# Performance work log

Hardware: AMD Instinct MI355X
Metric: run time of the kernel (lower is better)

The kernel has to match this reference:

```python
import jax, jax.numpy as jnp
import numpy as np

K = 20
EPS = 1e-5
NEG_SLOPE = 0.2


def knn_idx(x, k):
    # x: [B, C, N]; returns indices of k nearest neighbors [B, N, k]
    xx = jnp.sum(x * x, axis=1)                      # [B, N]
    inner = jnp.einsum('bcn,bcm->bnm', x, x)         # [B, N, N]
    neg_dist = 2.0 * inner - xx[:, :, None] - xx[:, None, :]
    return jax.lax.top_k(neg_dist, k)[1]             # [B, N, k]


def graph_feature(x, k):
    # x: [B, C, N] -> [B, 2C, N, k]
    idx = knn_idx(x, k)
    xT = jnp.transpose(x, (0, 2, 1))                 # [B, N, C]
    nbrs = jax.vmap(lambda feats, ids: feats[ids])(xT, idx)   # [B, N, k, C]
    ctr = jnp.broadcast_to(xT[:, :, None, :], nbrs.shape)
    feat = jnp.concatenate([nbrs - ctr, ctr], axis=-1)        # [B, N, k, 2C]
    return jnp.transpose(feat, (0, 3, 1, 2))


def bn(x, g, b, axes):
    # training-mode batchnorm over `axes`, channel dim = 1
    m = jnp.mean(x, axis=axes, keepdims=True)
    v = jnp.var(x, axis=axes, keepdims=True)
    shape = [1] * x.ndim
    shape[1] = -1
    g = g.reshape(shape)
    b = b.reshape(shape)
    return g * (x - m) * jax.lax.rsqrt(v + EPS) + b


def lrelu(x):
    return jax.nn.leaky_relu(x, NEG_SLOPE)


def setup_inputs() -> dict:
    key = jax.random.key(0)
    ks = jax.random.split(key, 4)
    x = jax.random.normal(ks[0], (4, 16, 512, 3), dtype=jnp.float32)
    w1 = jax.random.normal(ks[1], (64, 6), dtype=jnp.float32) * 0.1
    w2 = jax.random.normal(ks[2], (256, 128), dtype=jnp.float32) * 0.05
    w3 = jax.random.normal(ks[3], (512, 320), dtype=jnp.float32) * 0.05
    ones = jnp.ones
    zeros = jnp.zeros
    return {
        'x': x,
        'w1': w1, 'g1': ones(64, jnp.float32), 'b1': zeros(64, jnp.float32),
        'w2': w2, 'g2': ones(256, jnp.float32), 'b2': zeros(256, jnp.float32),
        'w3': w3, 'g3': ones(512, jnp.float32), 'b3': zeros(512, jnp.float32),
    }


def reference(x, w1, g1, b1, w2, g2, b2, w3, g3, b3):
    B, P, N, D = x.shape
    xp = jnp.transpose(x.reshape(B * P, N, D), (0, 2, 1))    # [BP, 3, N]

    f = graph_feature(xp, K)                                  # [BP, 6, N, K]
    h = lrelu(bn(jnp.einsum('bcnk,oc->bonk', f, w1), g1, b1, (0, 2, 3)))
    x1 = jnp.max(h, axis=-1)                                  # [BP, 64, N]

    f = graph_feature(x1, K)                                  # [BP, 128, N, K]
    h = lrelu(bn(jnp.einsum('bcnk,oc->bonk', f, w2), g2, b2, (0, 2, 3)))
    x2 = jnp.max(h, axis=-1)                                  # [BP, 256, N]

    cat = jnp.concatenate([x1, x2], axis=1)                   # [BP, 320, N]
    h = lrelu(bn(jnp.einsum('bcn,oc->bon', cat, w3), g3, b3, (0, 2)))  # [BP, 512, N]

    pooled = jnp.concatenate([jnp.max(h, axis=-1), jnp.mean(h, axis=-1)], axis=1)  # [BP, 1024]
    return pooled.reshape(B, P, -1)
```

## Files before the change

### kernel.cpp

```cpp
#include <hip/hip_runtime.h>
#include <hip/hip_bf16.h>
#include <math.h>

#define NBP 64
#define NP  512
#define KK  20

using short8 = __attribute__((ext_vector_type(8))) short;
using f32x4  = __attribute__((ext_vector_type(4))) float;

constexpr size_t O_X1   = 0;
constexpr size_t O_XCH  = 8388608;
constexpr size_t O_XCL  = 29360128;
constexpr size_t O_D    = 50331648;
constexpr size_t O_IDX  = 117440512;
constexpr size_t O_XX2  = 120061952;
constexpr size_t O_WC   = 120193024;
constexpr size_t O_W3H  = 120324096;
constexpr size_t O_W3L  = 120651776;
constexpr size_t O_SC1  = 120979456;
constexpr size_t O_SC2  = 120979968;
constexpr size_t O_SC3  = 120982016;
constexpr size_t O_ST1  = 120986112;
constexpr size_t O_ST2  = 120994304;
constexpr size_t O_ST3  = 121125376;
constexpr size_t STATS_BYTES = 8192 + 131072 + 262144;

__global__ __launch_bounds__(256) void prepw_kernel(const float* __restrict__ w2,
                                                    const float* __restrict__ w3,
                                                    float* __restrict__ Wcat,
                                                    __hip_bfloat16* __restrict__ w3h,
                                                    __hip_bfloat16* __restrict__ w3l) {
    int i = blockIdx.x * 256 + threadIdx.x;
    if (i < 32768) {
        int c = i >> 9, q = i & 511;
        Wcat[i] = (q < 256) ? w2[q * 128 + c]
                            : (w2[(q - 256) * 128 + 64 + c] - w2[(q - 256) * 128 + c]);
    } else if (i < 32768 + 163840) {
        int j = i - 32768;
        float v = w3[j];
        __hip_bfloat16 h = __float2bfloat16(v);
        w3h[j] = h;
        w3l[j] = __float2bfloat16(v - __bfloat162float(h));
    }
}

__device__ __forceinline__ void wave_top20_set(const float v[8], int lane, int* __restrict__ outp) {
    unsigned u[8];
#pragma unroll
    for (int q = 0; q < 8; q++) {
        unsigned b = __float_as_uint(v[q]);
        u[q] = (b & 0x80000000u) ? ~b : (b | 0x80000000u);
    }
    unsigned T = 0u;
    for (int b = 31; b >= 0; b--) {
        unsigned cand = T | (1u << b);
        int cnt = 0;
#pragma unroll
        for (int q = 0; q < 8; q++)
            cnt += __popcll(__ballot(u[q] >= cand));
        if (cnt >= KK) T = cand;
    }
    unsigned long long lmask = (1ull << lane) - 1ull;
    int slotbase = 0;
#pragma unroll
    for (int q = 0; q < 8; q++) {
        unsigned long long bgt = __ballot(u[q] > T);
        if (u[q] > T) {
            int slot = slotbase + __popcll(bgt & lmask);
            outp[slot] = lane + (q << 6);
        }
        slotbase += __popcll(bgt);
    }
    int need = KK - slotbase;
#pragma unroll
    for (int q = 0; q < 8; q++) {
        if (need > 0) {
            unsigned long long beq = __ballot(u[q] == T);
            int cq = __popcll(beq);
            int take = need < cq ? need : cq;
            if (u[q] == T) {
                int p = __popcll(beq & lmask);
                if (p < take) outp[slotbase + p] = lane + (q << 6);
            }
            slotbase += take;
            need -= take;
        }
    }
}

__global__ __launch_bounds__(256) void knn1_kernel(const float* __restrict__ x, int* __restrict__ idx1) {
    __shared__ float px[NP * 3];
    __shared__ float sxx[NP];
    int bp = blockIdx.x >> 7;
    int pg = blockIdx.x & 127;
    int wid = threadIdx.x >> 6;
    int lane = threadIdx.x & 63;
    int n = pg * 4 + wid;
    const float* xb = x + (size_t)bp * NP * 3;
    for (int i = threadIdx.x; i < NP * 3; i += 256) px[i] = xb[i];
    __syncthreads();
    for (int i = threadIdx.x; i < NP; i += 256) {
        float a = px[i * 3], b = px[i * 3 + 1], c = px[i * 3 + 2];
        sxx[i] = a * a + b * b + c * c;
    }
    __syncthreads();
    float rn0 = px[n * 3], rn1 = px[n * 3 + 1], rn2 = px[n * 3 + 2];
    float xxn = sxx[n];
    float v[8];
#pragma unroll
    for (int q = 0; q < 8; q++) {
        int m = lane + (q << 6);
        float dot = rn0 * px[m * 3] + rn1 * px[m * 3 + 1] + rn2 * px[m * 3 + 2];
        v[q] = 2.0f * dot - xxn - sxx[m];
    }
    wave_top20_set(v, lane, idx1 + ((size_t)bp * NP + n) * KK);
}

__global__ __launch_bounds__(256) void conv1_kernel(const float* __restrict__ x, const float* __restrict__ w1,
                                                    const int* __restrict__ idx1,
                                                    float* __restrict__ h1max, float* __restrict__ h1min,
                                                    double* __restrict__ stats1) {
    __shared__ double red1[4][64][2];
    int bp = blockIdx.x >> 5;
    int nt = blockIdx.x & 31;
    int n0 = nt * 16;
    int o  = threadIdx.x & 63;
    int nq = threadIdx.x >> 6;
    const float* xb = x + (size_t)bp * NP * 3;
    float w[6];
#pragma unroll
    for (int c = 0; c < 6; c++) w[c] = w1[o * 6 + c];
    double s = 0.0, s2 = 0.0;
    float omx[4], omn[4];
#pragma unroll
    for (int nn = 0; nn < 4; nn++) {
        int n = n0 + nq * 4 + nn;
        float c0 = xb[n * 3], c1 = xb[n * 3 + 1], c2 = xb[n * 3 + 2];
        const int* ip = idx1 + ((size_t)bp * NP + n) * KK;
        float mx = -INFINITY, mn = INFINITY;
        for (int k = 0; k < KK; k++) {
            int j = ip[k];
            float e0 = xb[j * 3], e1 = xb[j * 3 + 1], e2 = xb[j * 3 + 2];
            float h = w[0] * (e0 - c0) + w[1] * (e1 - c1) + w[2] * (e2 - c2)
                    + w[3] * c0 + w[4] * c1 + w[5] * c2;
            mx = fmaxf(mx, h); mn = fminf(mn, h);
            s += (double)h; s2 += (double)h * (double)h;
        }
        omx[nn] = mx; omn[nn] = mn;
    }
    size_t base = ((size_t)bp * 64 + o) * NP + n0 + nq * 4;
    *(float4*)&h1max[base] = make_float4(omx[0], omx[1], omx[2], omx[3]);
    *(float4*)&h1min[base] = make_float4(omn[0], omn[1], omn[2], omn[3]);
    red1[nq][o][0] = s; red1[nq][o][1] = s2;
    __syncthreads();
    if (threadIdx.x < 64) {
        int oo = threadIdx.x;
        double S = 0, S2 = 0;
        for (int q = 0; q < 4; q++) { S += red1[q][oo][0]; S2 += red1[q][oo][1]; }
        int copy = blockIdx.x & 7;
        atomicAdd(&stats1[(copy * 64 + oo) * 2], S);
        atomicAdd(&stats1[(copy * 64 + oo) * 2 + 1], S2);
    }
}

__global__ __launch_bounds__(256) void fprep_kernel(const double* __restrict__ stats, int ncopy, int nch,
                                                    double invN, const float* __restrict__ g,
                                                    const float* __restrict__ b, float* __restrict__ scsh) {
    int o = blockIdx.x * 256 + threadIdx.x;
    if (o >= nch) return;
    double S = 0, S2 = 0;
    for (int c = 0; c < ncopy; c++) {
        S  += stats[((size_t)c * nch + o) * 2];
        S2 += stats[((size_t)c * nch + o) * 2 + 1];
    }
    double m = S * invN;
    double v = S2 * invN - m * m;
    double sc = (double)g[o] / sqrt(v + 1e-5);
    scsh[o * 2]     = (float)sc;
    scsh[o * 2 + 1] = (float)((double)b[o] - sc * m);
}

__global__ __launch_bounds__(256) void fin1_kernel(const float* __restrict__ h1max, const float* __restrict__ h1min,
                                                   const float* __restrict__ scsh,
                                                   float* __restrict__ x1,
                                                   __hip_bfloat16* __restrict__ XCh,
                                                   __hip_bfloat16* __restrict__ XCl) {
    __shared__ float tile[64][33];
    int bp = blockIdx.x >> 4, nt = blockIdx.x & 15, n0 = nt * 32;
    for (int i = threadIdx.x; i < 64 * 32; i += 256) {
        int o = i >> 5, nl = i & 31;
        float sc = scsh[o * 2], sh = scsh[o * 2 + 1];
        size_t gi = ((size_t)bp * 64 + o) * NP + n0 + nl;
        float v = (sc >= 0.0f) ? h1max[gi] : h1min[gi];
        float y = sc * v + sh;
        y = (y >= 0.0f) ? y : 0.2f * y;
        x1[gi] = y;
        tile[o][nl] = y;
    }
    __syncthreads();
    for (int i = threadIdx.x; i < 64 * 32; i += 256) {
        int nl = i >> 6, o = i & 63;
        float y = tile[o][nl];
        __hip_bfloat16 h = __float2bfloat16(y);
        size_t base = ((size_t)bp * NP + n0 + nl) * 320 + o;
        XCh[base] = h;
        XCl[base] = __float2bfloat16(y - __bfloat162float(h));
    }
}

__global__ __launch_bounds__(256) void xx2_kernel(const float* __restrict__ x1, float* __restrict__ xx2v) {
    int i = blockIdx.x * 256 + threadIdx.x;
    int bp = i >> 9, n = i & 511;
    const float* xb = x1 + (size_t)bp * 64 * NP + n;
    float acc = 0.0f;
    for (int c = 0; c < 64; c++) { float v = xb[c * NP]; acc += v * v; }
    xx2v[i] = acc;
}

__global__ __launch_bounds__(256) void gram_kernel(const float* __restrict__ x1, const float* __restrict__ xx2v,
                                                   float* __restrict__ Dm) {
    __shared__ float An[64 * 128];
    __shared__ float Bm[64 * 128];
    int bp = blockIdx.x >> 4;
    int ntb = (blockIdx.x >> 2) & 3, mtb = blockIdx.x & 3;
    int n0 = ntb * 128, m0 = mtb * 128;
    const float* xb = x1 + (size_t)bp * 64 * NP;
    for (int i = threadIdx.x; i < 64 * 128; i += 256) {
        int c = i >> 7, r = i & 127;
        An[i] = xb[c * NP + n0 + r];
        Bm[i] = xb[c * NP + m0 + r];
    }
    __syncthreads();
    int ng = threadIdx.x & 15, mg = threadIdx.x >> 4;
    float acc[8][8];
#pragma unroll
    for (int r = 0; r < 8; r++)
#pragma unroll
        for (int j = 0; j < 8; j++) acc[r][j] = 0.0f;
    const float* ap = An + ng * 8;
    const float* bq = Bm + mg * 8;
#pragma unroll 2
    for (int c = 0; c < 64; c++) {
        float4 a0 = *(const float4*)(ap + c * 128);
        float4 a1 = *(const float4*)(ap + c * 128 + 4);
        float4 b0 = *(const float4*)(bq + c * 128);
        float4 b1 = *(const float4*)(bq + c * 128 + 4);
        float av[8] = {a0.x, a0.y, a0.z, a0.w, a1.x, a1.y, a1.z, a1.w};
        float bv[8] = {b0.x, b0.y, b0.z, b0.w, b1.x, b1.y, b1.z, b1.w};
#pragma unroll
        for (int r = 0; r < 8; r++)
#pragma unroll
            for (int j = 0; j < 8; j++) acc[r][j] += av[r] * bv[j];
    }
    float xm[8];
#pragma unroll
    for (int j = 0; j < 8; j++) xm[j] = xx2v[bp * NP + m0 + mg * 8 + j];
#pragma unroll
    for (int r = 0; r < 8; r++) {
        float xxn = xx2v[bp * NP + n0 + ng * 8 + r];
        float out[8];
#pragma unroll
        for (int j = 0; j < 8; j++) out[j] = 2.0f * acc[r][j] - xxn - xm[j];
        size_t base = ((size_t)bp * NP + n0 + ng * 8 + r) * NP + m0 + mg * 8;
        *(float4*)&Dm[base]     = make_float4(out[0], out[1], out[2], out[3]);
        *(float4*)&Dm[base + 4] = make_float4(out[4], out[5], out[6], out[7]);
    }
}

__global__ __launch_bounds__(256) void topk2_kernel(const float* __restrict__ Dm, int* __restrict__ idx2) {
    int wid = threadIdx.x >> 6;
    int lane = threadIdx.x & 63;
    int row = blockIdx.x * 4 + wid;
    const float* dr = Dm + (size_t)row * NP;
    float v[8];
#pragma unroll
    for (int q = 0; q < 8; q++) v[q] = dr[lane + (q << 6)];
    wave_top20_set(v, lane, idx2 + (size_t)row * KK);
}

__global__ __launch_bounds__(256) void conv2a_kernel(const float* __restrict__ x1, const float* __restrict__ Wcat,
                                                     float* __restrict__ Aout, float* __restrict__ Dtout) {
    __shared__ float An[64 * 128];
    __shared__ float Bm[64 * 128];
    int bp = blockIdx.x >> 4;
    int ntb = (blockIdx.x >> 2) & 3, qtb = blockIdx.x & 3;
    int n0 = ntb * 128, q0 = qtb * 128;
    const float* xb = x1 + (size_t)bp * 64 * NP;
    for (int i = threadIdx.x; i < 64 * 128; i += 256) {
        int c = i >> 7, r = i & 127;
        An[i] = xb[c * NP + n0 + r];
        Bm[i] = Wcat[c * 512 + q0 + r];
    }
    __syncthreads();
    int ng = threadIdx.x & 15, mg = threadIdx.x >> 4;
    float acc[8][8];
#pragma unroll
    for (int r = 0; r < 8; r++)
#pragma unroll
        for (int j = 0; j < 8; j++) acc[r][j] = 0.0f;
    const float* ap = An + ng * 8;
    const float* bq = Bm + mg * 8;
#pragma unroll 2
    for (int c = 0; c < 64; c++) {
        float4 a0 = *(const float4*)(ap + c * 128);
        float4 a1 = *(const float4*)(ap + c * 128 + 4);
        float4 b0 = *(const float4*)(bq + c * 128);
        float4 b1 = *(const float4*)(bq + c * 128 + 4);
        float av[8] = {a0.x, a0.y, a0.z, a0.w, a1.x, a1.y, a1.z, a1.w};
        float bv[8] = {b0.x, b0.y, b0.z, b0.w, b1.x, b1.y, b1.z, b1.w};
#pragma unroll
        for (int r = 0; r < 8; r++)
#pragma unroll
            for (int j = 0; j < 8; j++) acc[r][j] += av[r] * bv[j];
    }
    float* ob = (q0 < 256) ? Aout : Dtout;
    int qoff = (q0 & 255) + mg * 8;
#pragma unroll
    for (int r = 0; r < 8; r++) {
        size_t base = ((size_t)bp * NP + n0 + ng * 8 + r) * 256 + qoff;
        *(float4*)&ob[base]     = make_float4(acc[r][0], acc[r][1], acc[r][2], acc[r][3]);
        *(float4*)&ob[base + 4] = make_float4(acc[r][4], acc[r][5], acc[r][6], acc[r][7]);
    }
}

__global__ __launch_bounds__(256) void conv2b_kernel(const float* __restrict__ A, const float* __restrict__ Dt,
                                                     const int* __restrict__ idx2,
                                                     double* __restrict__ stats2) {
    __shared__ float Al[512 * 16];
    __shared__ double red[16][16][2];
    int bid = blockIdx.x;
    int bp = bid >> 5;
    int ot = (bid >> 1) & 15, nh = bid & 1;
    int o0 = ot * 16, n0 = nh * 256;
    int tid = threadIdx.x;
    for (int i = tid; i < 2048; i += 256) {
        int j = i >> 2, p = i & 3;
        *(float4*)&Al[j * 16 + p * 4] = *(const float4*)&A[((size_t)bp * NP + j) * 256 + o0 + p * 4];
    }
    __syncthreads();
    int o = tid & 15, np = tid >> 4;
    double sh = 0.0, sh2 = 0.0;
    for (int nn = 0; nn < 16; nn++) {
        int n = n0 + np * 16 + nn;
        const int* ip = idx2 + ((size_t)bp * NP + n) * KK;
        int4 ia = *(const int4*)ip, ib = *(const int4*)(ip + 4), ic = *(const int4*)(ip + 8);
        int4 id4 = *(const int4*)(ip + 12), ie = *(const int4*)(ip + 16);
        int js[20] = {ia.x, ia.y, ia.z, ia.w, ib.x, ib.y, ib.z, ib.w, ic.x, ic.y, ic.z, ic.w,
                      id4.x, id4.y, id4.z, id4.w, ie.x, ie.y, ie.z, ie.w};
        float dv = Dt[((size_t)bp * NP + n) * 256 + o0 + o];
        float s1 = 0.0f, s2 = 0.0f;
#pragma unroll
        for (int k = 0; k < KK; k++) {
            float a = Al[js[k] * 16 + o];
            s1 += a; s2 += a * a;
        }
        sh  += (double)s1 + 20.0 * (double)dv;
        sh2 += (double)s2 + 2.0 * (double)dv * (double)s1 + 20.0 * (double)dv * (double)dv;
    }
    red[np][o][0] = sh; red[np][o][1] = sh2;
    __syncthreads();
    if (tid < 16) {
        double S = 0, S2 = 0;
        for (int q = 0; q < 16; q++) { S += red[q][tid][0]; S2 += red[q][tid][1]; }
        int copy = bid & 31;
        atomicAdd(&stats2[(copy * 256 + o0 + tid) * 2], S);
        atomicAdd(&stats2[(copy * 256 + o0 + tid) * 2 + 1], S2);
    }
}

__global__ __launch_bounds__(256) void fin2g_kernel(const float* __restrict__ A, const float* __restrict__ Dt,
                                                    const int* __restrict__ idx2,
                                                    const float* __restrict__ scsh,
                                                    __hip_bfloat16* __restrict__ XCh,
                                                    __hip_bfloat16* __restrict__ XCl) {
    __shared__ float Al[512 * 16];
    int bid = blockIdx.x;
    int bp = bid >> 5;
    int ot = (bid >> 1) & 15, nh = bid & 1;
    int o0 = ot * 16, n0 = nh * 256;
    int tid = threadIdx.x;
    for (int i = tid; i < 2048; i += 256) {
        int j = i >> 2, p = i & 3;
        *(float4*)&Al[j * 16 + p * 4] = *(const float4*)&A[((size_t)bp * NP + j) * 256 + o0 + p * 4];
    }
    __syncthreads();
    int o = tid & 15, np = tid >> 4;
    float sc = scsh[(o0 + o) * 2], shift = scsh[(o0 + o) * 2 + 1];
    for (int nn = 0; nn < 16; nn++) {
        int n = n0 + np * 16 + nn;
        const int* ip = idx2 + ((size_t)bp * NP + n) * KK;
        int4 ia = *(const int4*)ip, ib = *(const int4*)(ip + 4), ic = *(const int4*)(ip + 8);
        int4 id4 = *(const int4*)(ip + 12), ie = *(const int4*)(ip + 16);
        int js[20] = {ia.x, ia.y, ia.z, ia.w, ib.x, ib.y, ib.z, ib.w, ic.x, ic.y, ic.z, ic.w,
                      id4.x, id4.y, id4.z, id4.w, ie.x, ie.y, ie.z, ie.w};
        float dv = Dt[((size_t)bp * NP + n) * 256 + o0 + o];
        float mx = -INFINITY, mn = INFINITY;
#pragma unroll
        for (int k = 0; k < KK; k++) {
            float a = Al[js[k] * 16 + o];
            mx = fmaxf(mx, a); mn = fminf(mn, a);
        }
        float v = ((sc >= 0.0f) ? mx : mn) + dv;
        float y = sc * v + shift;
        y = (y >= 0.0f) ? y : 0.2f * y;
        __hip_bfloat16 h = __float2bfloat16(y);
        size_t base = ((size_t)bp * NP + n) * 320 + 64 + o0 + o;
        XCh[base] = h;
        XCl[base] = __float2bfloat16(y - __bfloat162float(h));
    }
}

__global__ __launch_bounds__(256) void conv3m_kernel(const __hip_bfloat16* __restrict__ XCh,
                                                     const __hip_bfloat16* __restrict__ XCl,
                                                     const __hip_bfloat16* __restrict__ w3h,
                                                     const __hip_bfloat16* __restrict__ w3l,
                                                     float* __restrict__ h3,
                                                     double* __restrict__ stats3) {
    __shared__ __align__(16) __hip_bfloat16 smem3[384 * 64];
    int bid = blockIdx.x;
    int bp = bid >> 5, ot = (bid >> 3) & 3, nt = bid & 7;
    int o0 = ot * 128, n0 = nt * 64;
    int tid = threadIdx.x, l = tid & 63, w = tid >> 6;
    int wo = (w >> 1) * 64, wn = (w & 1) * 32;
    int lrow = l & 15, lj = l >> 4;
    f32x4 z4 = {0.f, 0.f, 0.f, 0.f};
    f32x4 acc[4][2];
#pragma unroll
    for (int mt = 0; mt < 4; mt++) { acc[mt][0] = z4; acc[mt][1] = z4; }
    for (int ct = 0; ct < 5; ct++) {
        int c0 = ct * 64;
        __syncthreads();
        float4 vals[12];
#pragma unroll
        for (int t = 0; t < 12; t++) {
            int i = tid + t * 256;
            int row = i >> 3, ch = i & 7;
            const __hip_bfloat16* src;
            if (row < 128)      src = w3h + (size_t)(o0 + row) * 320;
            else if (row < 256) src = w3l + (size_t)(o0 + row - 128) * 320;
            else if (row < 320) src = XCh + ((size_t)bp * NP + n0 + row - 256) * 320;
            else                src = XCl + ((size_t)bp * NP + n0 + row - 320) * 320;
            vals[t] = *(const float4*)(src + c0 + ch * 8);
        }
#pragma unroll
        for (int t = 0; t < 12; t++) {
            int i = tid + t * 256;
            int row = i >> 3, ch = i & 7;
            *(float4*)(smem3 + row * 64 + ((ch ^ (row & 7)) * 8)) = vals[t];
        }
        __syncthreads();
#pragma unroll
        for (int ks = 0; ks < 2; ks++) {
            short8 ah[4], al[4], bh[2], bl[2];
#pragma unroll
            for (int t = 0; t < 4; t++) {
                int r = wo + t * 16 + lrow;
                int c = (lj + 4 * ks) ^ (r & 7);
                ah[t] = *(const short8*)(smem3 + r * 64 + c * 8);
                al[t] = *(const short8*)(smem3 + (128 + r) * 64 + c * 8);
            }
#pragma unroll
            for (int t = 0; t < 2; t++) {
                int r = wn + t * 16 + lrow;
                int c = (lj + 4 * ks) ^ (r & 7);
                bh[t] = *(const short8*)(smem3 + (256 + r) * 64 + c * 8);
                bl[t] = *(const short8*)(smem3 + (320 + r) * 64 + c * 8);
            }
#pragma unroll
            for (int mt = 0; mt < 4; mt++)
#pragma unroll
                for (int nl = 0; nl < 2; nl++) {
                    acc[mt][nl] = __builtin_amdgcn_mfma_f32_16x16x32_bf16(al[mt], bh[nl], acc[mt][nl], 0, 0, 0);
                    acc[mt][nl] = __builtin_amdgcn_mfma_f32_16x16x32_bf16(ah[mt], bl[nl], acc[mt][nl], 0, 0, 0);
                    acc[mt][nl] = __builtin_amdgcn_mfma_f32_16x16x32_bf16(ah[mt], bh[nl], acc[mt][nl], 0, 0, 0);
                }
        }
    }
    __syncthreads();
    double* redD = (double*)smem3;
    size_t hb = (size_t)bp * 512;
#pragma unroll
    for (int mt = 0; mt < 4; mt++) {
#pragma unroll
        for (int rg = 0; rg < 4; rg++) {
            int ol = wo + mt * 16 + lj * 4 + rg;
            double s = 0.0, s2 = 0.0;
#pragma unroll
            for (int nl = 0; nl < 2; nl++) {
                float h = acc[mt][nl][rg];
                int ng = n0 + wn + nl * 16 + lrow;
                h3[(hb + o0 + ol) * 512 + ng] = h;
                s += (double)h; s2 += (double)h * (double)h;
            }
#pragma unroll
            for (int off = 1; off < 16; off <<= 1) {
                s  += __shfl_xor(s, off);
                s2 += __shfl_xor(s2, off);
            }
            if (lrow == 0) {
                redD[((w & 1) * 128 + ol) * 2]     = s;
                redD[((w & 1) * 128 + ol) * 2 + 1] = s2;
            }
        }
    }
    __syncthreads();
    if (tid < 128) {
        double S  = redD[tid * 2]     + redD[(128 + tid) * 2];
        double S2 = redD[tid * 2 + 1] + redD[(128 + tid) * 2 + 1];
        int copy = bid & 31;
        atomicAdd(&stats3[(copy * 512 + o0 + tid) * 2], S);
        atomicAdd(&stats3[(copy * 512 + o0 + tid) * 2 + 1], S2);
    }
}

__global__ __launch_bounds__(256) void pool_kernel(const float* __restrict__ h3, const float* __restrict__ scsh3,
                                                   float* __restrict__ out) {
    int row = blockIdx.x * 4 + (threadIdx.x >> 6);
    int lane = threadIdx.x & 63;
    int bp = row >> 9, o = row & 511;
    float sc = scsh3[o * 2], sh = scsh3[o * 2 + 1];
    const float* hr = h3 + (size_t)row * NP;
    float4 v0 = *(const float4*)&hr[lane * 4];
    float4 v1 = *(const float4*)&hr[256 + lane * 4];
    float vs[8] = {v0.x, v0.y, v0.z, v0.w, v1.x, v1.y, v1.z, v1.w};
    float mx = -INFINITY, sm = 0.0f;
#pragma unroll
    for (int q = 0; q < 8; q++) {
        float y = sc * vs[q] + sh;
        y = (y >= 0.0f) ? y : 0.2f * y;
        mx = fmaxf(mx, y); sm += y;
    }
    for (int off = 32; off >= 1; off >>= 1) {
        mx = fmaxf(mx, __shfl_xor(mx, off));
        sm += __shfl_xor(sm, off);
    }
    if (lane == 0) {
        out[(size_t)bp * 1024 + o]       = mx;
        out[(size_t)bp * 1024 + 512 + o] = sm * (1.0f / 512.0f);
    }
}

extern "C" void kernel_launch(void* const* d_in, const int* in_sizes, int n_in,
                              void* d_out, int out_size, void* d_ws, size_t ws_size,
                              hipStream_t stream) {
    const float* x  = (const float*)d_in[0];
    const float* w1 = (const float*)d_in[1];
    const float* g1 = (const float*)d_in[2];
    const float* b1 = (const float*)d_in[3];
    const float* w2 = (const float*)d_in[4];
    const float* g2 = (const float*)d_in[5];
    const float* b2 = (const float*)d_in[6];
    const float* w3 = (const float*)d_in[7];
    const float* g3 = (const float*)d_in[8];
    const float* b3 = (const float*)d_in[9];
    float* out = (float*)d_out;
    char* ws = (char*)d_ws;

    float*          x1    = (float*)(ws + O_X1);
    __hip_bfloat16* XCh   = (__hip_bfloat16*)(ws + O_XCH);
    __hip_bfloat16* XCl   = (__hip_bfloat16*)(ws + O_XCL);
    float*          Dbuf  = (float*)(ws + O_D);
    int*            idx   = (int*)(ws + O_IDX);
    float*          xx2v  = (float*)(ws + O_XX2);
    float*          Wcat  = (float*)(ws + O_WC);
    __hip_bfloat16* w3h   = (__hip_bfloat16*)(ws + O_W3H);
    __hip_bfloat16* w3l   = (__hip_bfloat16*)(ws + O_W3L);
    float*          scsh1 = (float*)(ws + O_SC1);
    float*          scsh2 = (float*)(ws + O_SC2);
    float*          scsh3 = (float*)(ws + O_SC3);
    double*         st1   = (double*)(ws + O_ST1);
    double*         st2   = (double*)(ws + O_ST2);
    double*         st3   = (double*)(ws + O_ST3);

    float* h1max = Dbuf;
    float* h1min = Dbuf + 2097152;
    float* Abuf  = Dbuf;
    float* Dt    = Dbuf + 8388608;
    float* h3    = Dbuf;

    hipMemsetAsync(ws + O_ST1, 0, STATS_BYTES, stream);
    prepw_kernel<<<768, 256, 0, stream>>>(w2, w3, Wcat, w3h, w3l);
    knn1_kernel<<<8192, 256, 0, stream>>>(x, idx);
    conv1_kernel<<<2048, 256, 0, stream>>>(x, w1, idx, h1max, h1min, st1);
    fprep_kernel<<<1, 256, 0, stream>>>(st1, 8, 64, 1.0 / 655360.0, g1, b1, scsh1);
    fin1_kernel<<<1024, 256, 0, stream>>>(h1max, h1min, scsh1, x1, XCh, XCl);
    xx2_kernel<<<128, 256, 0, stream>>>(x1, xx2v);
    gram_kernel<<<1024, 256, 0, stream>>>(x1, xx2v, Dbuf);
    topk2_kernel<<<8192, 256, 0, stream>>>(Dbuf, idx);
    conv2a_kernel<<<1024, 256, 0, stream>>>(x1, Wcat, Abuf, Dt);
    conv2b_kernel<<<2048, 256, 0, stream>>>(Abuf, Dt, idx, st2);
    fprep_kernel<<<1, 256, 0, stream>>>(st2, 32, 256, 1.0 / 655360.0, g2, b2, scsh2);
    fin2g_kernel<<<2048, 256, 0, stream>>>(Abuf, Dt, idx, scsh2, XCh, XCl);
    conv3m_kernel<<<2048, 256, 0, stream>>>(XCh, XCl, w3h, w3l, h3, st3);
    fprep_kernel<<<2, 256, 0, stream>>>(st3, 32, 512, 1.0 / 32768.0, g3, b3, scsh3);
    pool_kernel<<<8192, 256, 0, stream>>>(h3, scsh3, out);
}
```

Baseline: 466.6 us.

## Enlarge conv3 GEMM n-tile and load tiles via direct global-to-LDS

The conv3 split-bf16 MFMA kernel now computes 128x128 output tiles per block instead of 128x64, halving the grid and increasing per-wave accumulator count to 4x4. Tile loads use global_load_lds to write straight into shared memory, with the swizzle moved onto the global source address, bypassing registers. This aims to cut redundant weight loads and the register staging cost, at the price of more LDS, more accumulator registers and fewer blocks for occupancy.

```diff
diff --git a/kernel.cpp b/kernel.cpp
--- a/kernel.cpp
+++ b/kernel.cpp
@@ -26,6 +26,11 @@
 constexpr size_t O_ST3  = 121125376;
 constexpr size_t STATS_BYTES = 8192 + 131072 + 262144;
 
+__device__ __forceinline__ void gload_lds16(const void* g, void* l) {
+    __builtin_amdgcn_global_load_lds((const __attribute__((address_space(1))) unsigned int*)g,
+                                     (__attribute__((address_space(3))) unsigned int*)l, 16, 0, 0);
+}
+
 __global__ __launch_bounds__(256) void prepw_kernel(const float* __restrict__ w2,
                                                     const float* __restrict__ w3,
                                                     float* __restrict__ Wcat,
@@ -417,62 +422,55 @@
                                                      const __hip_bfloat16* __restrict__ w3l,
                                                      float* __restrict__ h3,
                                                      double* __restrict__ stats3) {
-    __shared__ __align__(16) __hip_bfloat16 smem3[384 * 64];
+    __shared__ __align__(16) __hip_bfloat16 smem3[512 * 64];
     int bid = blockIdx.x;
-    int bp = bid >> 5, ot = (bid >> 3) & 3, nt = bid & 7;
-    int o0 = ot * 128, n0 = nt * 64;
+    int bp = bid >> 4, ot = (bid >> 2) & 3, nt = bid & 3;
+    int o0 = ot * 128, n0 = nt * 128;
     int tid = threadIdx.x, l = tid & 63, w = tid >> 6;
-    int wo = (w >> 1) * 64, wn = (w & 1) * 32;
+    int wo = (w >> 1) * 64, wn = (w & 1) * 64;
     int lrow = l & 15, lj = l >> 4;
     f32x4 z4 = {0.f, 0.f, 0.f, 0.f};
-    f32x4 acc[4][2];
-#pragma unroll
-    for (int mt = 0; mt < 4; mt++) { acc[mt][0] = z4; acc[mt][1] = z4; }
+    f32x4 acc[4][4];
+#pragma unroll
+    for (int mt = 0; mt < 4; mt++)
+#pragma unroll
+        for (int nl = 0; nl < 4; nl++) acc[mt][nl] = z4;
     for (int ct = 0; ct < 5; ct++) {
         int c0 = ct * 64;
         __syncthreads();
-        float4 vals[12];
-#pragma unroll
-        for (int t = 0; t < 12; t++) {
-            int i = tid + t * 256;
-            int row = i >> 3, ch = i & 7;
-            const __hip_bfloat16* src;
-            if (row < 128)      src = w3h + (size_t)(o0 + row) * 320;
-            else if (row < 256) src = w3l + (size_t)(o0 + row - 128) * 320;
-            else if (row < 320) src = XCh + ((size_t)bp * NP + n0 + row - 256) * 320;
-            else                src = XCl + ((size_t)bp * NP + n0 + row - 320) * 320;
-            vals[t] = *(const float4*)(src + c0 + ch * 8);
-        }
-#pragma unroll
-        for (int t = 0; t < 12; t++) {
-            int i = tid + t * 256;
-            int row = i >> 3, ch = i & 7;
-            *(float4*)(smem3 + row * 64 + ((ch ^ (row & 7)) * 8)) = vals[t];
+#pragma unroll
+        for (int g = 0; g < 16; g++) {
+            int grp = w * 16 + g;
+            int row = grp * 8 + (l >> 3);
+            int ch  = l & 7;
+            const __hip_bfloat16* srcrow;
+            if (row < 128)      srcrow = w3h + (size_t)(o0 + row) * 320;
+            else if (row < 256) srcrow = w3l + (size_t)(o0 + row - 128) * 320;
+            else if (row < 384) srcrow = XCh + ((size_t)bp * NP + n0 + row - 256) * 320;
+            else                srcrow = XCl + ((size_t)bp * NP + n0 + row - 384) * 320;
+            gload_lds16(srcrow + c0 + ((ch ^ (row & 7)) * 8), smem3 + grp * 512);
         }
         __syncthreads();
 #pragma unroll
         for (int ks = 0; ks < 2; ks++) {
-            short8 ah[4], al[4], bh[2], bl[2];
+            short8 ah[4], alo[4], bh[4], blo[4];
 #pragma unroll
             for (int t = 0; t < 4; t++) {
                 int r = wo + t * 16 + lrow;
                 int c = (lj + 4 * ks) ^ (r & 7);
-                ah[t] = *(const short8*)(smem3 + r * 64 + c * 8);
-                al[t] = *(const short8*)(smem3 + (128 + r) * 64 + c * 8);
+                ah[t]  = *(const short8*)(smem3 + r * 64 + c * 8);
+                alo[t] = *(const short8*)(smem3 + (128 + r) * 64 + c * 8);
+                int r2 = wn + t * 16 + lrow;
+                int c2 = (lj + 4 * ks) ^ (r2 & 7);
+                bh[t]  = *(const short8*)(smem3 + (256 + r2) * 64 + c2 * 8);
+                blo[t] = *(const short8*)(smem3 + (384 + r2) * 64 + c2 * 8);
             }
 #pragma unroll
-            for (int t = 0; t < 2; t++) {
-                int r = wn + t * 16 + lrow;
-                int c = (lj + 4 * ks) ^ (r & 7);
-                bh[t] = *(const short8*)(smem3 + (256 + r) * 64 + c * 8);
-                bl[t] = *(const short8*)(smem3 + (320 + r) * 64 + c * 8);
-            }
-#pragma unroll
             for (int mt = 0; mt < 4; mt++)
 #pragma unroll
-                for (int nl = 0; nl < 2; nl++) {
-                    acc[mt][nl] = __builtin_amdgcn_mfma_f32_16x16x32_bf16(al[mt], bh[nl], acc[mt][nl], 0, 0, 0);
-                    acc[mt][nl] = __builtin_amdgcn_mfma_f32_16x16x32_bf16(ah[mt], bl[nl], acc[mt][nl], 0, 0, 0);
+                for (int nl = 0; nl < 4; nl++) {
+                    acc[mt][nl] = __builtin_amdgcn_mfma_f32_16x16x32_bf16(alo[mt], bh[nl], acc[mt][nl], 0, 0, 0);
+                    acc[mt][nl] = __builtin_amdgcn_mfma_f32_16x16x32_bf16(ah[mt], blo[nl], acc[mt][nl], 0, 0, 0);
                     acc[mt][nl] = __builtin_amdgcn_mfma_f32_16x16x32_bf16(ah[mt], bh[nl], acc[mt][nl], 0, 0, 0);
                 }
         }
@@ -487,7 +485,7 @@
             int ol = wo + mt * 16 + lj * 4 + rg;
             double s = 0.0, s2 = 0.0;
 #pragma unroll
-            for (int nl = 0; nl < 2; nl++) {
+            for (int nl = 0; nl < 4; nl++) {
                 float h = acc[mt][nl][rg];
                 int ng = n0 + wn + nl * 16 + lrow;
                 h3[(hb + o0 + ol) * 512 + ng] = h;
@@ -592,7 +590,7 @@
     conv2b_kernel<<<2048, 256, 0, stream>>>(Abuf, Dt, idx, st2);
     fprep_kernel<<<1, 256, 0, stream>>>(st2, 32, 256, 1.0 / 655360.0, g2, b2, scsh2);
     fin2g_kernel<<<2048, 256, 0, stream>>>(Abuf, Dt, idx, scsh2, XCh, XCl);
-    conv3m_kernel<<<2048, 256, 0, stream>>>(XCh, XCl, w3h, w3l, h3, st3);
+    conv3m_kernel<<<1024, 256, 0, stream>>>(XCh, XCl, w3h, w3l, h3, st3);
     fprep_kernel<<<2, 256, 0, stream>>>(st3, 32, 512, 1.0 / 32768.0, g3, b3, scsh3);
     pool_kernel<<<8192, 256, 0, stream>>>(h3, scsh3, out);
 }
```

New measurement: 475.4 us. About the same (+1.9%).
